# Kernel optimization log

Hardware: AMD Instinct MI355X
Metric: run time of the kernel (lower is better)

The kernel has to match this reference:

```python
import jax, jax.numpy as jnp
import numpy as np

NUM_EMBEDDINGS = 1024
EMBEDDING_DIM = 128
COMMITMENT_COST = 0.25
TOP_K = 3


def setup_inputs() -> dict:
    key = jax.random.key(0)
    k1, k2 = jax.random.split(key)
    inputs = jax.random.normal(k1, (32, 128, 32, 32), dtype=jnp.float32)
    embedding = jax.random.normal(k2, (NUM_EMBEDDINGS, EMBEDDING_DIM), dtype=jnp.float32)
    return {"inputs": inputs, "embedding": embedding}


def reference(inputs, embedding):
    # NCHW -> NHWC, flatten to [N, D]
    x = jnp.transpose(inputs, (0, 2, 3, 1))  # [B,H,W,D]
    input_shape = x.shape
    flat = x.reshape(-1, EMBEDDING_DIM)  # [N, D]

    # Squared L2 distances via GEMM: [N, K]
    distances = (
        jnp.sum(flat * flat, axis=1, keepdims=True)
        + jnp.sum(embedding * embedding, axis=1)
        - 2.0 * flat @ embedding.T
    )

    # top-k SMALLEST distances -> top_k of negated distances
    _, top_k_indices = jax.lax.top_k(-distances, TOP_K)  # [N, TOP_K]

    # Gather quantized vectors for all k at once: [N, TOP_K, D]
    quant_all = embedding[top_k_indices]
    # reshape per-k to input_shape -> [TOP_K, B, H, W, D]
    quant_k = jnp.transpose(quant_all, (1, 0, 2)).reshape((TOP_K,) + input_shape)

    # Torch loop leaves `encodings` = one-hot of the LAST (k-th nearest) index
    encodings = jax.nn.one_hot(top_k_indices[:, -1], NUM_EMBEDDINGS, dtype=jnp.float32)  # [N, K]

    q0 = quant_k[0]
    e_latent_loss = jnp.mean((jax.lax.stop_gradient(q0) - x) ** 2)
    loss = COMMITMENT_COST * e_latent_loss

    # Straight-through estimator
    quantized = x + jax.lax.stop_gradient(q0 - x)
    top_k_quantized = x[None] + jax.lax.stop_gradient(quant_k - x[None])  # [TOP_K,B,H,W,D]

    avg_probs = jnp.mean(encodings, axis=0)
    perplexity = jnp.exp(-jnp.sum(avg_probs * jnp.log(avg_probs + 1e-10)))

    quantized_nchw = jnp.transpose(quantized, (0, 3, 1, 2))
    return (loss, quantized_nchw, perplexity, encodings, top_k_quantized)
```

## Files before the change

### kernel.cpp

```cpp
#include <hip/hip_runtime.h>

#define BB 32
#define CC 128
#define HW 1024
#define NN 32768
#define KK 1024
#define DD 128
#define OFF_QUANT 1
#define OFF_PERP  4194305
#define OFF_ENC   4194306
#define OFF_TOPK  37748738

#define WS_PARTIALS 0
#define WS_HIST     32768
#define WS_TOP3     1085440
#define WS_EMBBF    1609728
#define WS_ENORM    1871872

typedef __attribute__((ext_vector_type(8))) short short8;
typedef __attribute__((ext_vector_type(4))) float f32x4;
typedef __attribute__((ext_vector_type(2))) float f32x2;

__device__ __forceinline__ ushort f32_to_bf16(float v) {
    uint u = __float_as_uint(v);
    u = (u + 0x7FFFu + ((u >> 16) & 1u)) >> 16;
    return (ushort)u;
}

__global__ __launch_bounds__(256) void kP_emb(
    const float* __restrict__ emb, ushort* __restrict__ embbf,
    float* __restrict__ enorm, int* __restrict__ hist)
{
    const int blk = blockIdx.x, t = threadIdx.x;
    const int rr = t >> 2, q = t & 3;
    const int row = blk * 64 + rr;
    const float4* src = (const float4*)(emb + (size_t)row * 128 + q * 32);
    short8* dst = (short8*)(embbf + (size_t)row * 128 + q * 32);
    float nrm = 0.f;
#pragma unroll
    for (int u2 = 0; u2 < 4; ++u2) {
        float4 a = src[u2 * 2], b2 = src[u2 * 2 + 1];
        float f[8] = {a.x, a.y, a.z, a.w, b2.x, b2.y, b2.z, b2.w};
        union { short8 v; ushort u[8]; } p;
#pragma unroll
        for (int j = 0; j < 8; ++j) {
            nrm = fmaf(f[j], f[j], nrm);
            p.u[j] = f32_to_bf16(f[j]);
        }
        dst[u2] = p.v;
    }
    nrm += __shfl_xor(nrm, 1);
    nrm += __shfl_xor(nrm, 2);
    if (q == 0) enorm[row] = nrm;
    if (blk == 0)
        for (int i = t; i < 1024; i += 256) hist[i] = 0;
}

__global__ __launch_bounds__(256) void kA2B(
    const float* __restrict__ in, const float* __restrict__ emb,
    const ushort* __restrict__ embbf, const float* __restrict__ enorm,
    int* __restrict__ top3, int* __restrict__ hist, double* __restrict__ partials)
{
    __shared__ union {
        float xs[128 * 66];
        uint4 et16[2048];
    } sh;
    __shared__ float enl[1024];
    __shared__ double lsum[64];
    __shared__ int cbuf[512];

    const int t = threadIdx.x;
    const int lane = t & 63, w = t >> 6;
    const int quad = lane >> 4, m = lane & 15;
    const int rowBase = blockIdx.x * 64;
    const int b = rowBase >> 10, hw0 = rowBase & 1023;
    const float* inB = in + (size_t)b * (CC * HW) + hw0;

    for (int i = t; i < 1024; i += 256) enl[i] = enorm[i];

    short8 A[4];
    {
        const int ra = w * 16 + m;
#pragma unroll
        for (int kk = 0; kk < 4; ++kk) {
            union { short8 v; ushort u[8]; } p;
#pragma unroll
            for (int j = 0; j < 8; ++j)
                p.u[j] = f32_to_bf16(inB[(size_t)(kk * 32 + quad * 8 + j) * HW + ra]);
            A[kk] = p.v;
        }
    }

    uint kq[4][3];
#pragma unroll
    for (int i = 0; i < 4; ++i)
        kq[i][0] = kq[i][1] = kq[i][2] = 0xFFFFFFFFu;

    const uint4* eg = (const uint4*)embbf;

    for (int tile = 0; tile < 8; ++tile) {
        __syncthreads();
#pragma unroll
        for (int u = 0; u < 8; ++u) {
            int c = u * 256 + t;
            int row = c >> 4, kb = c & 15;
            sh.et16[row * 16 + (kb ^ (row & 7))] = eg[(size_t)(tile * 128 + row) * 16 + kb];
        }
        __syncthreads();
#pragma unroll
        for (int sp = 0; sp < 4; ++sp) {
            f32x4 acc0 = {0.f, 0.f, 0.f, 0.f}, acc1 = {0.f, 0.f, 0.f, 0.f};
#pragma unroll
            for (int kk = 0; kk < 4; ++kk) {
                int sl = (kk * 4 + quad) ^ (m & 7);
                short8 B0 = *(const short8*)&sh.et16[((sp * 2)     * 16 + m) * 16 + sl];
                short8 B1 = *(const short8*)&sh.et16[((sp * 2 + 1) * 16 + m) * 16 + sl];
                acc0 = __builtin_amdgcn_mfma_f32_16x16x32_bf16(A[kk], B0, acc0, 0, 0, 0);
                acc1 = __builtin_amdgcn_mfma_f32_16x16x32_bf16(A[kk], B1, acc1, 0, 0, 0);
            }
            const int col0 = tile * 128 + (sp * 2) * 16 + m;
            const float en0 = enl[col0], en1 = enl[col0 + 16];
#pragma unroll
            for (int i = 0; i < 4; ++i) {
                {
                    float sc = fmaf(-2.f, acc0[i], en0);
                    uint u_ = __float_as_uint(sc);
                    u_ ^= (uint)(((int)u_) >> 31) | 0x80000000u;
                    uint key = (u_ & 0xFFFFFC00u) | (uint)col0;
                    uint t0 = max(kq[i][0], key); kq[i][0] = min(kq[i][0], key);
                    uint t1 = max(kq[i][1], t0);  kq[i][1] = min(kq[i][1], t0);
                    kq[i][2] = min(kq[i][2], t1);
                }
                {
                    float sc = fmaf(-2.f, acc1[i], en1);
                    uint u_ = __float_as_uint(sc);
                    u_ ^= (uint)(((int)u_) >> 31) | 0x80000000u;
                    uint key = (u_ & 0xFFFFFC00u) | (uint)(col0 + 16);
                    uint t0 = max(kq[i][0], key); kq[i][0] = min(kq[i][0], key);
                    uint t1 = max(kq[i][1], t0);  kq[i][1] = min(kq[i][1], t0);
                    kq[i][2] = min(kq[i][2], t1);
                }
            }
        }
    }

    __syncthreads();
    uint* keybuf = (uint*)sh.et16;
#pragma unroll
    for (int i = 0; i < 4; ++i) {
        int rowl = w * 16 + quad * 4 + i;
#pragma unroll
        for (int j = 0; j < 3; ++j)
            keybuf[(m * 3 + j) * 65 + rowl] = kq[i][j];
    }
    __syncthreads();

    if (t < 64) {
        uint D[8];
#pragma unroll
        for (int s = 0; s < 8; ++s) D[s] = 0xFFFFFFFFu;
        for (int s = 0; s < 48; ++s) {
            uint k = keybuf[s * 65 + t];
            if (k < D[7]) {
                D[7] = k;
#pragma unroll
                for (int u = 7; u > 0; --u)
                    if (D[u] < D[u - 1]) { uint tmp = D[u]; D[u] = D[u - 1]; D[u - 1] = tmp; }
            }
        }
#pragma unroll
        for (int s = 0; s < 8; ++s) cbuf[t * 8 + s] = (int)(D[s] & 1023u);
    }
    __syncthreads();

    for (int i = t; i < 8192; i += 256) {
        int c = i >> 6, r2 = i & 63;
        sh.xs[c * 66 + r2] = inB[(size_t)c * HW + r2];
    }
    __syncthreads();

    const int r = t >> 2;
    const int q = t & 3;
    const int n = rowBase + r;

    double dist[8]; int es[8];
#pragma unroll
    for (int s = 0; s < 8; ++s) {
        int e = cbuf[r * 8 + s];
        es[s] = e;
        const float4* er = (const float4*)(emb + (size_t)e * DD + q * 32);
        double acc = 0.0;
#pragma unroll
        for (int u = 0; u < 8; ++u) {
            float4 ev = er[u];
            int c0 = q * 32 + u * 4;
            double a0 = (double)sh.xs[(c0 + 0) * 66 + r] - (double)ev.x;
            double a1 = (double)sh.xs[(c0 + 1) * 66 + r] - (double)ev.y;
            double a2 = (double)sh.xs[(c0 + 2) * 66 + r] - (double)ev.z;
            double a3 = (double)sh.xs[(c0 + 3) * 66 + r] - (double)ev.w;
            acc += a0 * a0 + a1 * a1 + a2 * a2 + a3 * a3;
        }
        acc += __shfl_xor(acc, 1);
        acc += __shfl_xor(acc, 2);
        dist[s] = acc;
    }

    if (q == 0) {
        unsigned usedm = 0;
        int out_idx[3];
        double d_top1 = 0.0;
#pragma unroll
        for (int p = 0; p < 3; ++p) {
            double bd = 1.0e300; int bi = 0x7fffffff, bs = 0;
#pragma unroll
            for (int s = 0; s < 8; ++s) {
                if ((usedm >> s) & 1u) continue;
                if (dist[s] < bd || (dist[s] == bd && es[s] < bi)) {
                    bd = dist[s]; bi = es[s]; bs = s;
                }
            }
            usedm |= (1u << bs);
            out_idx[p] = bi;
            if (p == 0) d_top1 = bd;
        }
        top3[n * 4 + 0] = out_idx[0];
        top3[n * 4 + 1] = out_idx[1];
        top3[n * 4 + 2] = out_idx[2];
        atomicAdd(&hist[out_idx[2]], 1);
        lsum[r] = d_top1;
    }
    __syncthreads();
    if (t < 8) {
        double a = 0.0;
#pragma unroll
        for (int i2 = 0; i2 < 8; ++i2) a += lsum[t * 8 + i2];
        lsum[t] = a;
    }
    __syncthreads();
    if (t == 0) {
        double a = 0.0;
#pragma unroll
        for (int i2 = 0; i2 < 8; ++i2) a += lsum[i2];
        partials[blockIdx.x] = a;
    }
}

__global__ __launch_bounds__(256) void kEpi(
    const float* __restrict__ emb, const int* __restrict__ top3,
    const double* __restrict__ partials, const int* __restrict__ hist,
    float* __restrict__ out)
{
    __shared__ union {
        float cols[4][1024];
        int e8[8];
        double sred[256];
    } sh;
    const int blk = blockIdx.x, t = threadIdx.x;
    if (blk < 1024) {
        float* dst = out + OFF_QUANT;
        const int bb = blk >> 5;
        const int c0 = (4 * blk) & 127;
#pragma unroll
        for (int k = 0; k < 4; ++k) {
            int e = k * 256 + t;
            float4 f4 = *(const float4*)(emb + (size_t)e * DD + c0);
            sh.cols[0][e] = f4.x; sh.cols[1][e] = f4.y;
            sh.cols[2][e] = f4.z; sh.cols[3][e] = f4.w;
        }
        int e4[4];
#pragma unroll
        for (int v = 0; v < 4; ++v)
            e4[v] = top3[(bb * 1024 + v * 256 + t) * 4];
        __syncthreads();
#pragma unroll 4
        for (int u = 0; u < 16; ++u) {
            int j = blk * 4096 + u * 256 + t;
            dst[j] = sh.cols[u >> 2][e4[u & 3]];
        }
    } else if (blk < 4096) {
        const f32x2* e2 = (const f32x2*)emb;
        f32x2* dst = (f32x2*)(out + OFF_TOPK);
#pragma unroll 4
        for (int u = 0; u < 8; ++u) {
            int j  = (blk - 1024) * 2048 + u * 256 + t;
            int c2 = j & 63;
            int n  = (j >> 6) & 32767;
            int k  = j >> 21;
            int e  = top3[n * 4 + k];
            dst[j] = e2[e * 64 + c2];
        }
    } else if (blk < 8192) {
        const int row0 = (blk - 4096) * 8;
        if (t < 8) sh.e8[t] = top3[(row0 + t) * 4 + 2];
        __syncthreads();
        f32x2* dst = (f32x2*)(out + OFF_ENC) + (size_t)row0 * 512;
#pragma unroll 4
        for (int u = 0; u < 16; ++u) {
            int idx = u * 256 + t;
            int e = sh.e8[idx >> 9];
            int col = idx & 511;
            f32x2 v = {0.f, 0.f};
            if ((e >> 1) == col) v[e & 1] = 1.0f;
            dst[idx] = v;
        }
    } else {
        sh.sred[t] = partials[t] + partials[t + 256];
        __syncthreads();
        for (int s = 128; s > 0; s >>= 1) {
            if (t < s) sh.sred[t] += sh.sred[t + s];
            __syncthreads();
        }
        if (t == 0) out[0] = (float)(0.25 * sh.sred[0] / 4194304.0);
        __syncthreads();
        double s2 = 0.0;
#pragma unroll
        for (int i = 0; i < 4; ++i) {
            double p = (double)hist[t + i * 256] * (1.0 / 32768.0);
            s2 += p * log(p + 1e-10);
        }
        sh.sred[t] = s2;
        __syncthreads();
        for (int s = 128; s > 0; s >>= 1) {
            if (t < s) sh.sred[t] += sh.sred[t + s];
            __syncthreads();
        }
        if (t == 0) out[OFF_PERP] = (float)exp(-sh.sred[0]);
    }
}

extern "C" void kernel_launch(void* const* d_in, const int* in_sizes, int n_in,
                              void* d_out, int out_size, void* d_ws, size_t ws_size,
                              hipStream_t stream)
{
    const float* in  = (const float*)d_in[0];
    const float* emb = (const float*)d_in[1];
    float* out = (float*)d_out;
    char*  ws  = (char*)d_ws;

    double* partials = (double*)(ws + WS_PARTIALS);
    int*    hist     = (int*)(ws + WS_HIST);
    int*    top3     = (int*)(ws + WS_TOP3);
    ushort* embbf    = (ushort*)(ws + WS_EMBBF);
    float*  enorm    = (float*)(ws + WS_ENORM);

    kP_emb<<<dim3(16),   dim3(256), 0, stream>>>(emb, embbf, enorm, hist);
    kA2B  <<<dim3(512),  dim3(256), 0, stream>>>(in, emb, embbf, enorm, top3, hist, partials);
    kEpi  <<<dim3(8193), dim3(256), 0, stream>>>(emb, top3, partials, hist, out);
}
```

Before: 279.8 us.

## Fuse output scatter into distance kernel and stage input tile once in LDS

The separate epilogue kernel that wrote the quantized, top-k and one-hot outputs is folded into the main distance/top-k kernel, which now writes outputs straight from shared-memory top-3 indices. The global top3 buffer round trip and one large launch go away, and a tiny single-block kernel computes loss and perplexity. The input tile is loaded into LDS once up front and used for both the bf16 MFMA operands and the fp64 refinement, instead of being read from global twice. The cost is that the main kernel now holds more LDS (xs is no longer unioned), which may lower occupancy, and its 512 blocks must carry all the output bandwidth, so parallelism on the write phase drops.

```diff
diff --git a/kernel.cpp b/kernel.cpp
--- a/kernel.cpp
+++ b/kernel.cpp
@@ -13,7 +13,6 @@
 
 #define WS_PARTIALS 0
 #define WS_HIST     32768
-#define WS_TOP3     1085440
 #define WS_EMBBF    1609728
 #define WS_ENORM    1871872
 
@@ -56,18 +55,21 @@
         for (int i = t; i < 1024; i += 256) hist[i] = 0;
 }
 
-__global__ __launch_bounds__(256) void kA2B(
+__global__ __launch_bounds__(256) void kFull(
     const float* __restrict__ in, const float* __restrict__ emb,
     const ushort* __restrict__ embbf, const float* __restrict__ enorm,
-    int* __restrict__ top3, int* __restrict__ hist, double* __restrict__ partials)
+    int* __restrict__ hist, double* __restrict__ partials,
+    float* __restrict__ out)
 {
+    __shared__ float xs[128 * 66];
     __shared__ union {
-        float xs[128 * 66];
         uint4 et16[2048];
+        uint  kb[8192];
     } sh;
     __shared__ float enl[1024];
     __shared__ double lsum[64];
     __shared__ int cbuf[512];
+    __shared__ int s_top[3][64];
 
     const int t = threadIdx.x;
     const int lane = t & 63, w = t >> 6;
@@ -76,7 +78,12 @@
     const int b = rowBase >> 10, hw0 = rowBase & 1023;
     const float* inB = in + (size_t)b * (CC * HW) + hw0;
 
+    for (int i = t; i < 8192; i += 256) {
+        int c = i >> 6, r2 = i & 63;
+        xs[c * 66 + r2] = inB[(size_t)c * HW + r2];
+    }
     for (int i = t; i < 1024; i += 256) enl[i] = enorm[i];
+    __syncthreads();
 
     short8 A[4];
     {
@@ -86,7 +93,7 @@
             union { short8 v; ushort u[8]; } p;
 #pragma unroll
             for (int j = 0; j < 8; ++j)
-                p.u[j] = f32_to_bf16(inB[(size_t)(kk * 32 + quad * 8 + j) * HW + ra]);
+                p.u[j] = f32_to_bf16(xs[(kk * 32 + quad * 8 + j) * 66 + ra]);
             A[kk] = p.v;
         }
     }
@@ -103,8 +110,8 @@
 #pragma unroll
         for (int u = 0; u < 8; ++u) {
             int c = u * 256 + t;
-            int row = c >> 4, kb = c & 15;
-            sh.et16[row * 16 + (kb ^ (row & 7))] = eg[(size_t)(tile * 128 + row) * 16 + kb];
+            int row = c >> 4, kb2 = c & 15;
+            sh.et16[row * 16 + (kb2 ^ (row & 7))] = eg[(size_t)(tile * 128 + row) * 16 + kb2];
         }
         __syncthreads();
 #pragma unroll
@@ -145,13 +152,12 @@
     }
 
     __syncthreads();
-    uint* keybuf = (uint*)sh.et16;
 #pragma unroll
     for (int i = 0; i < 4; ++i) {
         int rowl = w * 16 + quad * 4 + i;
 #pragma unroll
         for (int j = 0; j < 3; ++j)
-            keybuf[(m * 3 + j) * 65 + rowl] = kq[i][j];
+            sh.kb[(m * 3 + j) * 65 + rowl] = kq[i][j];
     }
     __syncthreads();
 
@@ -160,7 +166,7 @@
 #pragma unroll
         for (int s = 0; s < 8; ++s) D[s] = 0xFFFFFFFFu;
         for (int s = 0; s < 48; ++s) {
-            uint k = keybuf[s * 65 + t];
+            uint k = sh.kb[s * 65 + t];
             if (k < D[7]) {
                 D[7] = k;
 #pragma unroll
@@ -170,12 +176,6 @@
         }
 #pragma unroll
         for (int s = 0; s < 8; ++s) cbuf[t * 8 + s] = (int)(D[s] & 1023u);
-    }
-    __syncthreads();
-
-    for (int i = t; i < 8192; i += 256) {
-        int c = i >> 6, r2 = i & 63;
-        sh.xs[c * 66 + r2] = inB[(size_t)c * HW + r2];
     }
     __syncthreads();
 
@@ -194,10 +194,10 @@
         for (int u = 0; u < 8; ++u) {
             float4 ev = er[u];
             int c0 = q * 32 + u * 4;
-            double a0 = (double)sh.xs[(c0 + 0) * 66 + r] - (double)ev.x;
-            double a1 = (double)sh.xs[(c0 + 1) * 66 + r] - (double)ev.y;
-            double a2 = (double)sh.xs[(c0 + 2) * 66 + r] - (double)ev.z;
-            double a3 = (double)sh.xs[(c0 + 3) * 66 + r] - (double)ev.w;
+            double a0 = (double)xs[(c0 + 0) * 66 + r] - (double)ev.x;
+            double a1 = (double)xs[(c0 + 1) * 66 + r] - (double)ev.y;
+            double a2 = (double)xs[(c0 + 2) * 66 + r] - (double)ev.z;
+            double a3 = (double)xs[(c0 + 3) * 66 + r] - (double)ev.w;
             acc += a0 * a0 + a1 * a1 + a2 * a2 + a3 * a3;
         }
         acc += __shfl_xor(acc, 1);
@@ -223,9 +223,9 @@
             out_idx[p] = bi;
             if (p == 0) d_top1 = bd;
         }
-        top3[n * 4 + 0] = out_idx[0];
-        top3[n * 4 + 1] = out_idx[1];
-        top3[n * 4 + 2] = out_idx[2];
+        s_top[0][r] = out_idx[0];
+        s_top[1][r] = out_idx[1];
+        s_top[2][r] = out_idx[2];
         atomicAdd(&hist[out_idx[2]], 1);
         lsum[r] = d_top1;
     }
@@ -243,89 +243,67 @@
         for (int i2 = 0; i2 < 8; ++i2) a += lsum[i2];
         partials[blockIdx.x] = a;
     }
-}
-
-__global__ __launch_bounds__(256) void kEpi(
-    const float* __restrict__ emb, const int* __restrict__ top3,
+
+    {
+        float* dq = out + OFF_QUANT + (size_t)b * (CC * HW) + hw0;
+        const int rq = t & 63, cg = t >> 6;
+        const float* erow = emb + (size_t)s_top[0][rq] * DD;
+#pragma unroll 8
+        for (int c = cg * 32; c < cg * 32 + 32; ++c)
+            dq[(size_t)c * HW + rq] = erow[c];
+    }
+    {
+        const f32x2* e2 = (const f32x2*)emb;
+        f32x2* dt = (f32x2*)(out + OFF_TOPK);
+#pragma unroll 4
+        for (int u = 0; u < 48; ++u) {
+            int idx = u * 256 + t;
+            int k  = idx >> 12;
+            int rr = (idx >> 6) & 63;
+            int c2 = idx & 63;
+            int e  = s_top[k][rr];
+            dt[(size_t)k * 2097152 + (size_t)(rowBase + rr) * 64 + c2] = e2[e * 64 + c2];
+        }
+    }
+    {
+        f32x2* de = (f32x2*)(out + OFF_ENC) + (size_t)rowBase * 512;
+        const f32x2 z = {0.f, 0.f};
+#pragma unroll 8
+        for (int u = 0; u < 128; ++u)
+            de[u * 256 + t] = z;
+    }
+    __syncthreads();
+    if (t < 64)
+        out[OFF_ENC + (size_t)(rowBase + t) * 1024 + s_top[2][t]] = 1.0f;
+}
+
+__global__ __launch_bounds__(256) void kFin(
     const double* __restrict__ partials, const int* __restrict__ hist,
     float* __restrict__ out)
 {
-    __shared__ union {
-        float cols[4][1024];
-        int e8[8];
-        double sred[256];
-    } sh;
-    const int blk = blockIdx.x, t = threadIdx.x;
-    if (blk < 1024) {
-        float* dst = out + OFF_QUANT;
-        const int bb = blk >> 5;
-        const int c0 = (4 * blk) & 127;
-#pragma unroll
-        for (int k = 0; k < 4; ++k) {
-            int e = k * 256 + t;
-            float4 f4 = *(const float4*)(emb + (size_t)e * DD + c0);
-            sh.cols[0][e] = f4.x; sh.cols[1][e] = f4.y;
-            sh.cols[2][e] = f4.z; sh.cols[3][e] = f4.w;
-        }
-        int e4[4];
-#pragma unroll
-        for (int v = 0; v < 4; ++v)
-            e4[v] = top3[(bb * 1024 + v * 256 + t) * 4];
+    __shared__ double sred[256];
+    const int t = threadIdx.x;
+    sred[t] = partials[t] + partials[t + 256];
+    __syncthreads();
+    for (int s = 128; s > 0; s >>= 1) {
+        if (t < s) sred[t] += sred[t + s];
         __syncthreads();
-#pragma unroll 4
-        for (int u = 0; u < 16; ++u) {
-            int j = blk * 4096 + u * 256 + t;
-            dst[j] = sh.cols[u >> 2][e4[u & 3]];
-        }
-    } else if (blk < 4096) {
-        const f32x2* e2 = (const f32x2*)emb;
-        f32x2* dst = (f32x2*)(out + OFF_TOPK);
-#pragma unroll 4
-        for (int u = 0; u < 8; ++u) {
-            int j  = (blk - 1024) * 2048 + u * 256 + t;
-            int c2 = j & 63;
-            int n  = (j >> 6) & 32767;
-            int k  = j >> 21;
-            int e  = top3[n * 4 + k];
-            dst[j] = e2[e * 64 + c2];
-        }
-    } else if (blk < 8192) {
-        const int row0 = (blk - 4096) * 8;
-        if (t < 8) sh.e8[t] = top3[(row0 + t) * 4 + 2];
+    }
+    if (t == 0) out[0] = (float)(0.25 * sred[0] / 4194304.0);
+    __syncthreads();
+    double s2 = 0.0;
+#pragma unroll
+    for (int i = 0; i < 4; ++i) {
+        double p = (double)hist[t + i * 256] * (1.0 / 32768.0);
+        s2 += p * log(p + 1e-10);
+    }
+    sred[t] = s2;
+    __syncthreads();
+    for (int s = 128; s > 0; s >>= 1) {
+        if (t < s) sred[t] += sred[t + s];
         __syncthreads();
-        f32x2* dst = (f32x2*)(out + OFF_ENC) + (size_t)row0 * 512;
-#pragma unroll 4
-        for (int u = 0; u < 16; ++u) {
-            int idx = u * 256 + t;
-            int e = sh.e8[idx >> 9];
-            int col = idx & 511;
-            f32x2 v = {0.f, 0.f};
-            if ((e >> 1) == col) v[e & 1] = 1.0f;
-            dst[idx] = v;
-        }
-    } else {
-        sh.sred[t] = partials[t] + partials[t + 256];
-        __syncthreads();
-        for (int s = 128; s > 0; s >>= 1) {
-            if (t < s) sh.sred[t] += sh.sred[t + s];
-            __syncthreads();
-        }
-        if (t == 0) out[0] = (float)(0.25 * sh.sred[0] / 4194304.0);
-        __syncthreads();
-        double s2 = 0.0;
-#pragma unroll
-        for (int i = 0; i < 4; ++i) {
-            double p = (double)hist[t + i * 256] * (1.0 / 32768.0);
-            s2 += p * log(p + 1e-10);
-        }
-        sh.sred[t] = s2;
-        __syncthreads();
-        for (int s = 128; s > 0; s >>= 1) {
-            if (t < s) sh.sred[t] += sh.sred[t + s];
-            __syncthreads();
-        }
-        if (t == 0) out[OFF_PERP] = (float)exp(-sh.sred[0]);
-    }
+    }
+    if (t == 0) out[OFF_PERP] = (float)exp(-sred[0]);
 }
 
 extern "C" void kernel_launch(void* const* d_in, const int* in_sizes, int n_in,
@@ -339,11 +317,10 @@
 
     double* partials = (double*)(ws + WS_PARTIALS);
     int*    hist     = (int*)(ws + WS_HIST);
-    int*    top3     = (int*)(ws + WS_TOP3);
     ushort* embbf    = (ushort*)(ws + WS_EMBBF);
     float*  enorm    = (float*)(ws + WS_ENORM);
 
-    kP_emb<<<dim3(16),   dim3(256), 0, stream>>>(emb, embbf, enorm, hist);
-    kA2B  <<<dim3(512),  dim3(256), 0, stream>>>(in, emb, embbf, enorm, top3, hist, partials);
-    kEpi  <<<dim3(8193), dim3(256), 0, stream>>>(emb, top3, partials, hist, out);
-}
+    kP_emb<<<dim3(16),  dim3(256), 0, stream>>>(emb, embbf, enorm, hist);
+    kFull <<<dim3(512), dim3(256), 0, stream>>>(in, emb, embbf, enorm, hist, partials, out);
+    kFin  <<<dim3(1),   dim3(256), 0, stream>>>(partials, hist, out);
+}
```

Result: faster. 266.7 us (-4.7%).
